# Kernel optimization log

Hardware: AMD Instinct MI355X
Metric: run time of the kernel (lower is better)

Reference implementation:

```python
import jax, jax.numpy as jnp
import numpy as np

K = 3       # kernel size
PAD = 1
IMG = 512   # hard-coded img_size in source
CIN = 32
COUT = 32
B = 1
NORI = 8    # output_stabilizer_size


def make_group_mask(size=IMG, n=NORI):
    # group_conv_8mask: partition image into 8 angular sectors around the
    # fisheye center -> one-hot [8, H, W] mask selecting one orientation per pixel.
    c = (size - 1) / 2.0
    yy, xx = np.meshgrid(np.arange(size), np.arange(size), indexing='ij')
    ang = np.arctan2(yy - c, xx - c)  # [-pi, pi]
    sector = (np.floor((ang + np.pi) / (2.0 * np.pi) * n).astype(np.int64)) % n
    m = np.zeros((n, size, size), np.float32)
    m[sector.reshape(-1), yy.reshape(-1), xx.reshape(-1)] = 1.0
    return m


def rotate_kernel(w, deg):
    # bilinear rotation of [..., K, K] kernel about its center, zero fill (TorchRotate)
    th = np.deg2rad(deg)
    c = (K - 1) / 2.0
    ii, jj = jnp.meshgrid(jnp.arange(K, dtype=jnp.float32), jnp.arange(K, dtype=jnp.float32), indexing='ij')
    cos, sin = np.cos(th).astype(np.float32), np.sin(th).astype(np.float32)
    ys = cos * (ii - c) + sin * (jj - c) + c   # inverse-rotated source coords
    xs = -sin * (ii - c) + cos * (jj - c) + c
    y0 = jnp.floor(ys); x0 = jnp.floor(xs)
    wy = ys - y0; wx = xs - x0
    out = jnp.zeros_like(w)
    for dy, wy_ in ((0, 1.0 - wy), (1, wy)):
        for dx, wx_ in ((0, 1.0 - wx), (1, wx)):
            iy = (y0 + dy).astype(jnp.int32); ix = (x0 + dx).astype(jnp.int32)
            valid = ((iy >= 0) & (iy < K) & (ix >= 0) & (ix < K)).astype(w.dtype)
            iyc = jnp.clip(iy, 0, K - 1); ixc = jnp.clip(ix, 0, K - 1)
            out = out + w[..., iyc, ixc] * (wy_ * wx_ * valid)
    return out


def conv2d(x, w, b):
    y = jax.lax.conv_general_dilated(x, w, (1, 1), ((PAD, PAD), (PAD, PAD)),
                                     dimension_numbers=('NCHW', 'OIHW', 'NCHW'))
    return y + b[None, :, None, None]


def bilinear_gather(x, py, px):
    # x: [Cin, H, W]; py/px: [KK, H, W] fractional sample coords (zero outside)
    H, W = x.shape[-2], x.shape[-1]
    y0 = jnp.floor(py); x0 = jnp.floor(px)
    wy = py - y0; wx = px - x0
    out = jnp.zeros((x.shape[0],) + py.shape, x.dtype)
    for dy, wy_ in ((0, 1.0 - wy), (1, wy)):
        for dx, wx_ in ((0, 1.0 - wx), (1, wx)):
            iy = (y0 + dy).astype(jnp.int32); ix = (x0 + dx).astype(jnp.int32)
            valid = ((iy >= 0) & (iy < H) & (ix >= 0) & (ix < W)).astype(x.dtype)
            iyc = jnp.clip(iy, 0, H - 1); ixc = jnp.clip(ix, 0, W - 1)
            g = x[:, iyc, ixc]  # [Cin, KK, H, W]
            out = out + g * (wy_ * wx_ * valid)[None]
    return out


def _forward(x, weight, offset_w, offset_b, mask_w, mask_b, group_mask):
    # --- group-equivariant weight transform: 8 orientations (0/90/180/270 + 45-rotated set)
    base = weight[:, :, 0]                                        # [Cout, Cin, K, K]
    rots = [jnp.rot90(base, k=r, axes=(-2, -1)) for r in range(4)]
    w45 = rotate_kernel(base, 45.0)
    rots45 = [jnp.rot90(w45, k=r, axes=(-2, -1)) for r in range(4)]
    tw = jnp.stack(rots + rots45, axis=1)                         # [Cout, 8, Cin, K, K]
    tw = tw.reshape(COUT * NORI, CIN, K * K)

    H, W = x.shape[-2], x.shape[-1]
    offset = conv2d(x, offset_w, offset_b)                        # [B, 2*KK, H, W]
    modm = conv2d(x, mask_w, mask_b)                              # [B, KK, H, W]
    offset = offset.at[:, 8:10].set(0.0)                          # center-tap offsets zeroed
    modm = jax.nn.sigmoid(modm.at[:, 4].set(0.0))                 # center-tap logit zeroed

    off = offset.reshape(B, K * K, 2, H, W)                       # (dy, dx) pairs per tap
    ky, kx = jnp.meshgrid(jnp.arange(K, dtype=x.dtype), jnp.arange(K, dtype=x.dtype), indexing='ij')
    py = jnp.arange(H, dtype=x.dtype)[None, :, None] - PAD + ky.reshape(-1, 1, 1)
    px = jnp.arange(W, dtype=x.dtype)[None, None, :] - PAD + kx.reshape(-1, 1, 1)
    py = py[None] + off[:, :, 0]                                  # [B, KK, H, W]
    px = px[None] + off[:, :, 1]

    sampled = jax.vmap(bilinear_gather)(x, py, px)                # [B, Cin, KK, H, W]
    sampled = sampled * modm[:, None]                             # modulation
    y = jnp.einsum('bckhw,ock->bohw', sampled, tw)                # [B, Cout*8, H, W]
    y = y.reshape(B, COUT, NORI, H, W)
    y = jax.nn.relu(y)
    y = y * group_mask[None, None]                                # adaptive pool is identity at stride 1
    return y.sum(axis=2)                                          # [B, Cout, H, W]


def setup_inputs() -> dict:
    key = jax.random.key(0)
    ks = jax.random.split(key, 6)
    stdv = float(1.0 / np.sqrt(CIN * K * K))
    return {
        'input': jax.random.normal(ks[0], (B, CIN, IMG, IMG), jnp.float32),
        'weight': jax.random.uniform(ks[1], (COUT, CIN, 1, K, K), jnp.float32, -stdv, stdv),
        'offset_w': jax.random.normal(ks[2], (2 * K * K, CIN, K, K), jnp.float32) * 0.01,
        'offset_b': jax.random.normal(ks[3], (2 * K * K,), jnp.float32) * 0.01,
        'mask_w': jax.random.normal(ks[4], (K * K, CIN, K, K), jnp.float32) * 0.01,
        'mask_b': jax.random.normal(ks[5], (K * K,), jnp.float32) * 0.01,
        'group_mask': jnp.asarray(make_group_mask()),
    }


def reference(input, weight, offset_w, offset_b, mask_w, mask_b, group_mask):
    return _forward(input, weight, offset_w, offset_b, mask_w, mask_b, group_mask)
```

## Files before the change

kernel.cpp:

```cpp
#include <hip/hip_runtime.h>

#define IMG 512
#define CIN 32
#define COUT 32
#define NORI 8
#define HW (IMG*IMG)

#define TS 16

#define W1 18
#define WR1 19
#define CHS1P 346
#define HALO 4
#define WIN 24
#define WROW 24
#define CHSP 578

typedef _Float16 h2 __attribute__((ext_vector_type(2)));
typedef __fp16  fp16v2 __attribute__((ext_vector_type(2)));
typedef _Float16 f16x8 __attribute__((ext_vector_type(8)));
typedef float    f32x4 __attribute__((ext_vector_type(4)));

__device__ __forceinline__ float dot2acc(unsigned int a, unsigned int b, float c) {
#if __has_builtin(__builtin_amdgcn_fdot2)
    return __builtin_amdgcn_fdot2(__builtin_bit_cast(h2, a),
                                  __builtin_bit_cast(h2, b), c, false);
#else
    h2 av = __builtin_bit_cast(h2, a), bv = __builtin_bit_cast(h2, b);
    return fmaf((float)av[0], (float)bv[0], fmaf((float)av[1], (float)bv[1], c));
#endif
}

__device__ __forceinline__ unsigned int packh2(float a, float b) {
#if __has_builtin(__builtin_amdgcn_cvt_pkrtz)
    fp16v2 r = __builtin_amdgcn_cvt_pkrtz(a, b);
    return __builtin_bit_cast(unsigned int, r);
#else
    h2 r; r[0] = (_Float16)a; r[1] = (_Float16)b;
    return __builtin_bit_cast(unsigned int, r);
#endif
}

__device__ __forceinline__ unsigned int packh2_rne(float a, float b) {
    h2 r; r[0] = (_Float16)a; r[1] = (_Float16)b;
    return __builtin_bit_cast(unsigned int, r);
}

#define GEMV8(TP, S2) do {                                             \
    const uint4* _tp = (TP);                                           \
    _Pragma("unroll")                                                  \
    for (int q = 0; q < 8; ++q) {                                      \
        uint4 u = _tp[q];                                              \
        oacc[q * 4 + 0] = dot2acc((S2), u.x, oacc[q * 4 + 0]);         \
        oacc[q * 4 + 1] = dot2acc((S2), u.y, oacc[q * 4 + 1]);         \
        oacc[q * 4 + 2] = dot2acc((S2), u.z, oacc[q * 4 + 2]);         \
        oacc[q * 4 + 3] = dot2acc((S2), u.w, oacc[q * 4 + 3]);         \
    }                                                                  \
} while (0)

__global__ void build_tw_kernel(const float* __restrict__ weight, unsigned int* __restrict__ tw_h) {
    int idx = blockIdx.x * blockDim.x + threadIdx.x;
    if (idx >= COUT * (CIN / 2)) return;
    int o = idx & 31, cp = idx >> 5;

    float bb[2][9], w45[2][9];
    const float cs = 0.70710678f;
#pragma unroll
    for (int h = 0; h < 2; ++h) {
        int c = 2 * cp + h;
#pragma unroll
        for (int t = 0; t < 9; ++t) bb[h][t] = weight[(o * CIN + c) * 9 + t];
#pragma unroll
        for (int i = 0; i < 3; ++i) {
#pragma unroll
            for (int j = 0; j < 3; ++j) {
                float ys = cs * (float)(i - 1) + cs * (float)(j - 1) + 1.0f;
                float xs = -cs * (float)(i - 1) + cs * (float)(j - 1) + 1.0f;
                float y0f = floorf(ys), x0f = floorf(xs);
                float wy = ys - y0f, wx = xs - x0f;
                int iy0 = (int)y0f, ix0 = (int)x0f;
                float a = 0.0f;
#pragma unroll
                for (int dy = 0; dy < 2; ++dy) {
#pragma unroll
                    for (int dx = 0; dx < 2; ++dx) {
                        int iy = iy0 + dy, ix = ix0 + dx;
                        float wgt = (dy ? wy : 1.0f - wy) * (dx ? wx : 1.0f - wx);
                        bool valid = (iy >= 0) && (iy < 3) && (ix >= 0) && (ix < 3);
                        int iyc = min(max(iy, 0), 2), ixc = min(max(ix, 0), 2);
                        a += bb[h][iyc * 3 + ixc] * (valid ? wgt : 0.0f);
                    }
                }
                w45[h][i * 3 + j] = a;
            }
        }
    }

#pragma unroll
    for (int r = 0; r < NORI; ++r) {
        int rr = r & 3;
#pragma unroll
        for (int i = 0; i < 3; ++i) {
#pragma unroll
            for (int j = 0; j < 3; ++j) {
                int si, sj;
                if (rr == 0) { si = i;     sj = j;     }
                else if (rr == 1) { si = j;     sj = 2 - i; }
                else if (rr == 2) { si = 2 - i; sj = 2 - j; }
                else { si = 2 - j; sj = i;     }
                float v0 = (r < 4) ? bb[0][si * 3 + sj] : w45[0][si * 3 + sj];
                float v1 = (r < 4) ? bb[1][si * 3 + sj] : w45[1][si * 3 + sj];
                tw_h[(((r * 9) + (i * 3 + j)) * (CIN / 2) + cp) * COUT + o] =
                    packh2_rne(v0, v1);
            }
        }
    }
}

__global__ void pack_owmb_kernel(const float* __restrict__ offw, const float* __restrict__ mskw,
                                 unsigned int* __restrict__ owmb) {
    int idx = blockIdx.x * blockDim.x + threadIdx.x;
    if (idx >= 9 * 16 * 32) return;
    int oc = idx & 31;
    int cp = (idx >> 5) & 15;
    int kt = idx >> 9;
    float v0 = 0.0f, v1 = 0.0f;
    if (oc < 18) {
        v0 = offw[(oc * CIN + 2 * cp) * 9 + kt];
        v1 = offw[(oc * CIN + 2 * cp + 1) * 9 + kt];
    } else if (oc < 27) {
        v0 = mskw[((oc - 18) * CIN + 2 * cp) * 9 + kt];
        v1 = mskw[((oc - 18) * CIN + 2 * cp + 1) * 9 + kt];
    }
    owmb[(kt * 16 + cp) * 32 + oc] = packh2_rne(v0, v1);
}

__global__ __launch_bounds__(256, 4) void offset_mask_mfma_kernel(
    const float* __restrict__ x,
    const unsigned int* __restrict__ owmb,
    const float* __restrict__ offb, const float* __restrict__ mskb,
    float* __restrict__ om)
{
    __shared__ unsigned int Lp[16 * CHS1P];

    const int tiles_x = IMG / TS;
    int bid = (int)blockIdx.x;
    bid = (bid % 8) * (1024 / 8) + bid / 8;
    int bx = bid % tiles_x, by = bid / tiles_x;
    int tid = threadIdx.x;
    int y0w = by * TS - 1, x0w = bx * TS - 1;

    for (int i = tid; i < 16 * (W1 * W1); i += 256) {
        int pr = i / (W1 * W1), cell = i % (W1 * W1);
        int rr = cell / W1, cc = cell % W1;
        int gy = y0w + rr, gx = x0w + cc;
        float a = 0.0f, b = 0.0f;
        if ((unsigned)gy < (unsigned)IMG && (unsigned)gx < (unsigned)IMG) {
            const float* x0 = x + (2 * pr) * HW + gy * IMG + gx;
            a = x0[0]; b = x0[HW];
        }
        Lp[pr * CHS1P + rr * WR1 + cc] = packh2_rne(a, b);
    }
    __syncthreads();

    int lane = tid & 63, wid = tid >> 6;
    int lrow = lane & 15, lhi = lane >> 4;

    f32x4 acc[4][2] = {};

#pragma unroll
    for (int kt = 0; kt < 9; ++kt) {
        const int ky = kt / 3, kx = kt % 3;
        const unsigned int* tb = owmb + (kt * 16 + lhi * 4) * 32 + lrow;
        unsigned int bu0[4], bu1[4];
#pragma unroll
        for (int jj = 0; jj < 4; ++jj) {
            bu0[jj] = tb[jj * 32];
            bu1[jj] = tb[jj * 32 + 16];
        }
        uint4 b0q = make_uint4(bu0[0], bu0[1], bu0[2], bu0[3]);
        uint4 b1q = make_uint4(bu1[0], bu1[1], bu1[2], bu1[3]);
        f16x8 bf0 = __builtin_bit_cast(f16x8, b0q);
        f16x8 bf1 = __builtin_bit_cast(f16x8, b1q);

#pragma unroll
        for (int mt = 0; mt < 4; ++mt) {
            int yy = wid * 4 + mt;
            int lq = (yy + ky) * WR1 + (lrow + kx);
            unsigned int au[4];
#pragma unroll
            for (int j = 0; j < 4; ++j)
                au[j] = Lp[(lhi * 4 + j) * CHS1P + lq];
            uint4 aq = make_uint4(au[0], au[1], au[2], au[3]);
            f16x8 af = __builtin_bit_cast(f16x8, aq);
            acc[mt][0] = __builtin_amdgcn_mfma_f32_16x16x32_f16(af, bf0, acc[mt][0], 0, 0, 0);
            acc[mt][1] = __builtin_amdgcn_mfma_f32_16x16x32_f16(af, bf1, acc[mt][1], 0, 0, 0);
        }
    }

    float bias_n0 = offb[lrow];
    float bias_n1 = (lrow < 2) ? offb[16 + lrow]
                  : ((lrow < 11) ? mskb[lrow - 2] : 0.0f);
    int Xs = bx * 16 + lhi * 4;
#pragma unroll
    for (int mt = 0; mt < 4; ++mt) {
        int Yg = by * 16 + wid * 4 + mt;
        {
            int oc = lrow;
            float* op = om + oc * HW + Yg * IMG + Xs;
            bool zero = (oc == 8) || (oc == 9);
#pragma unroll
            for (int q = 0; q < 4; ++q)
                op[q] = zero ? 0.0f : (acc[mt][0][q] + bias_n0);
        }
        {
            int oc = 16 + lrow;
            if (oc < 27) {
                float* op = om + oc * HW + Yg * IMG + Xs;
#pragma unroll
                for (int q = 0; q < 4; ++q) {
                    float t = acc[mt][1][q] + bias_n1;
                    if (oc >= 18) t = (oc == 22) ? 0.5f : 1.0f / (1.0f + __expf(-t));
                    op[q] = t;
                }
            }
        }
    }
}

__global__ __launch_bounds__(256, 4) void deform_mfma_kernel(
    const float* __restrict__ x,
    const float* __restrict__ om,
    const float* __restrict__ gm,
    const unsigned int* __restrict__ tw_h,
    float* __restrict__ out)
{
    __shared__ unsigned int Lx[16 * CHSP];
    __shared__ uint2 Wl[256];
    __shared__ unsigned int LQa[256];
    __shared__ int flags[2];

    const int tiles_x = IMG / TS;
    int bid = (int)blockIdx.x;
    bid = (bid % 8) * (1024 / 8) + bid / 8;
    int bx = bid % tiles_x, by = bid / tiles_x;
    int tid = threadIdx.x;
    int tx = tid & 15, ty = tid >> 4;
    int X = bx * TS + tx, Y = by * TS + ty;
    int p = Y * IMG + X;
    int y0w = by * TS - HALO, x0w = bx * TS - HALO;

    if (tid < 2) flags[tid] = 0;
    __syncthreads();

    for (int i = tid; i < 16 * (WIN * WIN); i += 256) {
        int pr = i / (WIN * WIN), cell = i % (WIN * WIN);
        int rr = cell / WIN, cc = cell % WIN;
        int gy = y0w + rr, gx = x0w + cc;
        float a = 0.0f, b = 0.0f;
        if ((unsigned)gy < (unsigned)IMG && (unsigned)gx < (unsigned)IMG) {
            const float* x0 = x + (2 * pr) * HW + gy * IMG + gx;
            a = x0[0]; b = x0[HW];
        }
        Lx[pr * CHSP + rr * WROW + cc] = packh2_rne(a, b);
    }

    int r = 0;
#pragma unroll
    for (int n = 1; n < NORI; ++n) r = (gm[n * HW + p] > 0.5f) ? n : r;

    bool slow = false;
    for (int kt = 0; kt < 9; ++kt) {
        int ky = kt / 3, kx = kt - ky * 3;
        float offy = om[(2 * kt) * HW + p];
        float offx = om[(2 * kt + 1) * HW + p];
        float pyf = (float)(Y - 1 + ky) + offy;
        float pxf = (float)(X - 1 + kx) + offx;
        int iy0 = (int)floorf(pyf), ix0 = (int)floorf(pxf);
        int ryu = iy0 - y0w, rxu = ix0 - x0w;
        slow |= !(((unsigned)ryu < (WIN - 1)) && ((unsigned)rxu < (WIN - 1)));
    }
    atomicOr(&flags[0], 1 << r);
    if (slow) flags[1] = 1;
    __syncthreads();

    int rmaskv = __builtin_amdgcn_readfirstlane(flags[0]);
    int anyslow = flags[1];

    if (anyslow) {
        float oacc[32];
#pragma unroll
        for (int o = 0; o < 32; ++o) oacc[o] = 0.0f;
        for (int kt = 0; kt < 9; ++kt) {
            int ky = kt / 3, kx = kt - ky * 3;
            float offy = om[(2 * kt) * HW + p];
            float offx = om[(2 * kt + 1) * HW + p];
            float m    = om[(18 + kt) * HW + p];
            float pyf = (float)(Y - 1 + ky) + offy;
            float pxf = (float)(X - 1 + kx) + offx;
            float y0f = floorf(pyf), x0f = floorf(pxf);
            float wy = pyf - y0f, wx = pxf - x0f;
            int iy0 = (int)y0f, ix0 = (int)x0f;
            float vy0 = ((unsigned)iy0 < (unsigned)IMG) ? 1.0f : 0.0f;
            float vy1 = ((unsigned)(iy0 + 1) < (unsigned)IMG) ? 1.0f : 0.0f;
            float vx0 = ((unsigned)ix0 < (unsigned)IMG) ? 1.0f : 0.0f;
            float vx1 = ((unsigned)(ix0 + 1) < (unsigned)IMG) ? 1.0f : 0.0f;
            float w00 = m * (1.0f - wy) * (1.0f - wx) * vy0 * vx0;
            float w01 = m * (1.0f - wy) * wx * vy0 * vx1;
            float w10 = m * wy * (1.0f - wx) * vy1 * vx0;
            float w11 = m * wy * wx * vy1 * vx1;
            int cy0 = min(max(iy0, 0), IMG - 1), cy1 = min(max(iy0 + 1, 0), IMG - 1);
            int cx0 = min(max(ix0, 0), IMG - 1), cx1 = min(max(ix0 + 1, 0), IMG - 1);
            int g00 = cy0 * IMG + cx0, g01 = cy0 * IMG + cx1;
            int g10 = cy1 * IMG + cx0, g11 = cy1 * IMG + cx1;
            const uint4* tp = (const uint4*)(tw_h + (unsigned)((r * 9 + kt) * (CIN / 2)) * COUT);
            for (int cp = 0; cp < CIN / 2; ++cp) {
                const float* xc0 = x + (2 * cp) * HW;
                const float* xc1 = xc0 + HW;
                float s0 = fmaf(w00, xc0[g00], fmaf(w01, xc0[g01],
                           fmaf(w10, xc0[g10], w11 * xc0[g11])));
                float s1 = fmaf(w00, xc1[g00], fmaf(w01, xc1[g01],
                           fmaf(w10, xc1[g10], w11 * xc1[g11])));
                unsigned int s2 = packh2(s0, s1);
                GEMV8(tp + cp * 8, s2);
            }
        }
#pragma unroll
        for (int o = 0; o < 32; ++o) out[o * HW + p] = fmaxf(oacc[o], 0.0f);
        return;
    }

    int lane = tid & 63, wid = tid >> 6;
    int lrow = lane & 15, lhi = lane >> 4;

    f32x4 acc[4][2] = {};

    for (int kt = 0; kt < 9; ++kt) {
        int ky = kt / 3, kx = kt - ky * 3;
        {
            float offy = om[(2 * kt) * HW + p];
            float offx = om[(2 * kt + 1) * HW + p];
            float m    = om[(18 + kt) * HW + p];
            float pyf = (float)(Y - 1 + ky) + offy;
            float pxf = (float)(X - 1 + kx) + offx;
            float y0f = floorf(pyf), x0f = floorf(pxf);
            float wy = pyf - y0f, wx = pxf - x0f;
            int iy0 = (int)y0f, ix0 = (int)x0f;
            float vy0 = ((unsigned)iy0 < (unsigned)IMG) ? 1.0f : 0.0f;
            float vy1 = ((unsigned)(iy0 + 1) < (unsigned)IMG) ? 1.0f : 0.0f;
            float vx0 = ((unsigned)ix0 < (unsigned)IMG) ? 1.0f : 0.0f;
            float vx1 = ((unsigned)(ix0 + 1) < (unsigned)IMG) ? 1.0f : 0.0f;
            float w00 = m * (1.0f - wy) * (1.0f - wx) * vy0 * vx0;
            float w01 = m * (1.0f - wy) * wx * vy0 * vx1;
            float w10 = m * wy * (1.0f - wx) * vy1 * vx0;
            float w11 = m * wy * wx * vy1 * vx1;
            Wl[tid]  = make_uint2(packh2_rne(w00, w01), packh2_rne(w10, w11));
            LQa[tid] = (unsigned)((iy0 - y0w) * WROW + (ix0 - x0w)) | ((unsigned)r << 12);
        }
        __syncthreads();

        int Rv[4];
        unsigned int sam[4][4];
#pragma unroll
        for (int mt = 0; mt < 4; ++mt) {
            int px = (wid * 4 + mt) * 16 + lrow;
            uint2 wv = Wl[px];
            unsigned lqr = LQa[px];
            h2 wpa = __builtin_bit_cast(h2, wv.x);
            h2 wpb = __builtin_bit_cast(h2, wv.y);
            h2 w00 = __builtin_shufflevector(wpa, wpa, 0, 0);
            h2 w01 = __builtin_shufflevector(wpa, wpa, 1, 1);
            h2 w10 = __builtin_shufflevector(wpb, wpb, 0, 0);
            h2 w11 = __builtin_shufflevector(wpb, wpb, 1, 1);
            int lq = (int)(lqr & 0xFFF);
            Rv[mt] = (int)(lqr >> 12);
#pragma unroll
            for (int j = 0; j < 4; ++j) {
                int lb = (lhi * 4 + j) * CHSP + lq;
                h2 v00 = __builtin_bit_cast(h2, Lx[lb]);
                h2 v01 = __builtin_bit_cast(h2, Lx[lb + 1]);
                h2 v10 = __builtin_bit_cast(h2, Lx[lb + WROW]);
                h2 v11 = __builtin_bit_cast(h2, Lx[lb + WROW + 1]);
                h2 s = w00 * v00 + w01 * v01 + w10 * v10 + w11 * v11;
                sam[mt][j] = __builtin_bit_cast(unsigned int, s);
            }
        }

        int rm = rmaskv;
        while (rm) {
            int rr = __ffs(rm) - 1;
            rm &= rm - 1;
            const unsigned int* tb = tw_h +
                (unsigned)((rr * 9 + kt) * (CIN / 2) + lhi * 4) * COUT + lrow;
            unsigned int bu0[4], bu1[4];
#pragma unroll
            for (int jj = 0; jj < 4; ++jj) {
                bu0[jj] = tb[jj * COUT];
                bu1[jj] = tb[jj * COUT + 16];
            }
            uint4 b0q = make_uint4(bu0[0], bu0[1], bu0[2], bu0[3]);
            uint4 b1q = make_uint4(bu1[0], bu1[1], bu1[2], bu1[3]);
            f16x8 bf0 = __builtin_bit_cast(f16x8, b0q);
            f16x8 bf1 = __builtin_bit_cast(f16x8, b1q);

#pragma unroll
            for (int mt = 0; mt < 4; ++mt) {
                unsigned int keep = (Rv[mt] == rr) ? 0xFFFFFFFFu : 0u;
                uint4 aq = make_uint4(sam[mt][0] & keep, sam[mt][1] & keep,
                                      sam[mt][2] & keep, sam[mt][3] & keep);
                f16x8 af = __builtin_bit_cast(f16x8, aq);
                acc[mt][0] = __builtin_amdgcn_mfma_f32_16x16x32_f16(af, bf0, acc[mt][0], 0, 0, 0);
                acc[mt][1] = __builtin_amdgcn_mfma_f32_16x16x32_f16(af, bf1, acc[mt][1], 0, 0, 0);
            }
        }
        __syncthreads();
    }

    int Xs = bx * 16 + lhi * 4;
#pragma unroll
    for (int mt = 0; mt < 4; ++mt) {
        int Yg = by * 16 + wid * 4 + mt;
#pragma unroll
        for (int nt = 0; nt < 2; ++nt) {
            float* op = out + (nt * 16 + lrow) * HW + Yg * IMG + Xs;
#pragma unroll
            for (int q = 0; q < 4; ++q)
                op[q] = fmaxf(acc[mt][nt][q], 0.0f);
        }
    }
}

extern "C" void kernel_launch(void* const* d_in, const int* in_sizes, int n_in,
                              void* d_out, int out_size, void* d_ws, size_t ws_size,
                              hipStream_t stream) {
    const float* x      = (const float*)d_in[0];
    const float* weight = (const float*)d_in[1];
    const float* offw   = (const float*)d_in[2];
    const float* offb   = (const float*)d_in[3];
    const float* mskw   = (const float*)d_in[4];
    const float* mskb   = (const float*)d_in[5];
    const float* gm     = (const float*)d_in[6];
    float* out = (float*)d_out;

    unsigned int* tw_h = (unsigned int*)d_ws;
    unsigned int* owmb = (unsigned int*)((char*)d_ws + 147456);
    float* om = (float*)((char*)d_ws + 294912);

    build_tw_kernel<<<2, 256, 0, stream>>>(weight, tw_h);
    pack_owmb_kernel<<<18, 256, 0, stream>>>(offw, mskw, owmb);

    const int tiles = (IMG / TS) * (IMG / TS);
    offset_mask_mfma_kernel<<<tiles, 256, 0, stream>>>(x, owmb, offb, mskb, om);
    deform_mfma_kernel<<<tiles, 256, 0, stream>>>(x, om, gm, tw_h, out);
}
```

Baseline: 84.10 us.

## Fuse offset/mask conv into deform kernel via shared-memory fp16 buffer

Merges the offset/mask MFMA convolution into the deformable conv kernel. The offset and mask values are computed from the input tile already staged in shared memory, then kept in LDS as fp16 instead of a 27-channel fp32 global buffer. This drops one kernel launch, the global write and read-back of the offset/mask tensor, and the second staging of the input halo. In exchange it uses more LDS per block, lowers launch bounds to 3 blocks per SIMD, and stores offsets at fp16 precision, which could shift sampling coordinates slightly.

```diff
diff --git a/kernel.cpp b/kernel.cpp
--- a/kernel.cpp
+++ b/kernel.cpp
@@ -8,9 +8,6 @@
 
 #define TS 16
 
-#define W1 18
-#define WR1 19
-#define CHS1P 346
 #define HALO 4
 #define WIN 24
 #define WROW 24
@@ -44,6 +41,14 @@
 __device__ __forceinline__ unsigned int packh2_rne(float a, float b) {
     h2 r; r[0] = (_Float16)a; r[1] = (_Float16)b;
     return __builtin_bit_cast(unsigned int, r);
+}
+
+__device__ __forceinline__ unsigned short f16bits(float v) {
+    _Float16 h = (_Float16)v;
+    return __builtin_bit_cast(unsigned short, h);
+}
+__device__ __forceinline__ float f16val(unsigned short u) {
+    return (float)__builtin_bit_cast(_Float16, u);
 }
 
 #define GEMV8(TP, S2) do {                                             \
@@ -135,107 +140,16 @@
     owmb[(kt * 16 + cp) * 32 + oc] = packh2_rne(v0, v1);
 }
 
-__global__ __launch_bounds__(256, 4) void offset_mask_mfma_kernel(
+__global__ __launch_bounds__(256, 3) void fused_deform_kernel(
     const float* __restrict__ x,
     const unsigned int* __restrict__ owmb,
     const float* __restrict__ offb, const float* __restrict__ mskb,
-    float* __restrict__ om)
-{
-    __shared__ unsigned int Lp[16 * CHS1P];
-
-    const int tiles_x = IMG / TS;
-    int bid = (int)blockIdx.x;
-    bid = (bid % 8) * (1024 / 8) + bid / 8;
-    int bx = bid % tiles_x, by = bid / tiles_x;
-    int tid = threadIdx.x;
-    int y0w = by * TS - 1, x0w = bx * TS - 1;
-
-    for (int i = tid; i < 16 * (W1 * W1); i += 256) {
-        int pr = i / (W1 * W1), cell = i % (W1 * W1);
-        int rr = cell / W1, cc = cell % W1;
-        int gy = y0w + rr, gx = x0w + cc;
-        float a = 0.0f, b = 0.0f;
-        if ((unsigned)gy < (unsigned)IMG && (unsigned)gx < (unsigned)IMG) {
-            const float* x0 = x + (2 * pr) * HW + gy * IMG + gx;
-            a = x0[0]; b = x0[HW];
-        }
-        Lp[pr * CHS1P + rr * WR1 + cc] = packh2_rne(a, b);
-    }
-    __syncthreads();
-
-    int lane = tid & 63, wid = tid >> 6;
-    int lrow = lane & 15, lhi = lane >> 4;
-
-    f32x4 acc[4][2] = {};
-
-#pragma unroll
-    for (int kt = 0; kt < 9; ++kt) {
-        const int ky = kt / 3, kx = kt % 3;
-        const unsigned int* tb = owmb + (kt * 16 + lhi * 4) * 32 + lrow;
-        unsigned int bu0[4], bu1[4];
-#pragma unroll
-        for (int jj = 0; jj < 4; ++jj) {
-            bu0[jj] = tb[jj * 32];
-            bu1[jj] = tb[jj * 32 + 16];
-        }
-        uint4 b0q = make_uint4(bu0[0], bu0[1], bu0[2], bu0[3]);
-        uint4 b1q = make_uint4(bu1[0], bu1[1], bu1[2], bu1[3]);
-        f16x8 bf0 = __builtin_bit_cast(f16x8, b0q);
-        f16x8 bf1 = __builtin_bit_cast(f16x8, b1q);
-
-#pragma unroll
-        for (int mt = 0; mt < 4; ++mt) {
-            int yy = wid * 4 + mt;
-            int lq = (yy + ky) * WR1 + (lrow + kx);
-            unsigned int au[4];
-#pragma unroll
-            for (int j = 0; j < 4; ++j)
-                au[j] = Lp[(lhi * 4 + j) * CHS1P + lq];
-            uint4 aq = make_uint4(au[0], au[1], au[2], au[3]);
-            f16x8 af = __builtin_bit_cast(f16x8, aq);
-            acc[mt][0] = __builtin_amdgcn_mfma_f32_16x16x32_f16(af, bf0, acc[mt][0], 0, 0, 0);
-            acc[mt][1] = __builtin_amdgcn_mfma_f32_16x16x32_f16(af, bf1, acc[mt][1], 0, 0, 0);
-        }
-    }
-
-    float bias_n0 = offb[lrow];
-    float bias_n1 = (lrow < 2) ? offb[16 + lrow]
-                  : ((lrow < 11) ? mskb[lrow - 2] : 0.0f);
-    int Xs = bx * 16 + lhi * 4;
-#pragma unroll
-    for (int mt = 0; mt < 4; ++mt) {
-        int Yg = by * 16 + wid * 4 + mt;
-        {
-            int oc = lrow;
-            float* op = om + oc * HW + Yg * IMG + Xs;
-            bool zero = (oc == 8) || (oc == 9);
-#pragma unroll
-            for (int q = 0; q < 4; ++q)
-                op[q] = zero ? 0.0f : (acc[mt][0][q] + bias_n0);
-        }
-        {
-            int oc = 16 + lrow;
-            if (oc < 27) {
-                float* op = om + oc * HW + Yg * IMG + Xs;
-#pragma unroll
-                for (int q = 0; q < 4; ++q) {
-                    float t = acc[mt][1][q] + bias_n1;
-                    if (oc >= 18) t = (oc == 22) ? 0.5f : 1.0f / (1.0f + __expf(-t));
-                    op[q] = t;
-                }
-            }
-        }
-    }
-}
-
-__global__ __launch_bounds__(256, 4) void deform_mfma_kernel(
-    const float* __restrict__ x,
-    const float* __restrict__ om,
     const float* __restrict__ gm,
     const unsigned int* __restrict__ tw_h,
     float* __restrict__ out)
 {
     __shared__ unsigned int Lx[16 * CHSP];
+    __shared__ unsigned short OMl[256 * 27];
     __shared__ uint2 Wl[256];
     __shared__ unsigned int LQa[256];
     __shared__ int flags[2];
@@ -251,7 +165,6 @@
     int y0w = by * TS - HALO, x0w = bx * TS - HALO;
 
     if (tid < 2) flags[tid] = 0;
-    __syncthreads();
 
     for (int i = tid; i < 16 * (WIN * WIN); i += 256) {
         int pr = i / (WIN * WIN), cell = i % (WIN * WIN);
@@ -264,6 +177,74 @@
         }
         Lx[pr * CHSP + rr * WROW + cc] = packh2_rne(a, b);
     }
+    __syncthreads();
+
+    int lane = tid & 63, wid = tid >> 6;
+    int lrow = lane & 15, lhi = lane >> 4;
+
+    {
+        f32x4 acc1[4][2] = {};
+#pragma unroll
+        for (int kt = 0; kt < 9; ++kt) {
+            const int ky = kt / 3, kx = kt % 3;
+            const unsigned int* tb = owmb + (kt * 16 + lhi * 4) * 32 + lrow;
+            unsigned int bu0[4], bu1[4];
+#pragma unroll
+            for (int jj = 0; jj < 4; ++jj) {
+                bu0[jj] = tb[jj * 32];
+                bu1[jj] = tb[jj * 32 + 16];
+            }
+            uint4 b0q = make_uint4(bu0[0], bu0[1], bu0[2], bu0[3]);
+            uint4 b1q = make_uint4(bu1[0], bu1[1], bu1[2], bu1[3]);
+            f16x8 bf0 = __builtin_bit_cast(f16x8, b0q);
+            f16x8 bf1 = __builtin_bit_cast(f16x8, b1q);
+
+#pragma unroll
+            for (int mt = 0; mt < 4; ++mt) {
+                int yy = wid * 4 + mt;
+                int lq1 = (yy + ky + 3) * WROW + (lrow + kx + 3);
+                unsigned int au[4];
+#pragma unroll
+                for (int j = 0; j < 4; ++j)
+                    au[j] = Lx[(lhi * 4 + j) * CHSP + lq1];
+                uint4 aq = make_uint4(au[0], au[1], au[2], au[3]);
+                f16x8 af = __builtin_bit_cast(f16x8, aq);
+                acc1[mt][0] = __builtin_amdgcn_mfma_f32_16x16x32_f16(af, bf0, acc1[mt][0], 0, 0, 0);
+                acc1[mt][1] = __builtin_amdgcn_mfma_f32_16x16x32_f16(af, bf1, acc1[mt][1], 0, 0, 0);
+            }
+        }
+
+        float bias_n0 = offb[lrow];
+        float bias_n1 = (lrow < 2) ? offb[16 + lrow]
+                      : ((lrow < 11) ? mskb[lrow - 2] : 0.0f);
+#pragma unroll
+        for (int mt = 0; mt < 4; ++mt) {
+            int py_l = wid * 4 + mt;
+            {
+                int oc = lrow;
+                bool zero = (oc == 8) || (oc == 9);
+#pragma unroll
+                for (int q = 0; q < 4; ++q) {
+                    int px_l = py_l * 16 + lhi * 4 + q;
+                    float v = zero ? 0.0f : (acc1[mt][0][q] + bias_n0);
+                    OMl[px_l * 27 + oc] = f16bits(v);
+                }
+            }
+            {
+                int oc = 16 + lrow;
+                if (oc < 27) {
+#pragma unroll
+                    for (int q = 0; q < 4; ++q) {
+                        int px_l = py_l * 16 + lhi * 4 + q;
+                        float t = acc1[mt][1][q] + bias_n1;
+                        if (oc >= 18) t = (oc == 22) ? 0.5f : 1.0f / (1.0f + __expf(-t));
+                        OMl[px_l * 27 + oc] = f16bits(t);
+                    }
+                }
+            }
+        }
+    }
+    __syncthreads();
 
     int r = 0;
 #pragma unroll
@@ -272,8 +253,8 @@
     bool slow = false;
     for (int kt = 0; kt < 9; ++kt) {
         int ky = kt / 3, kx = kt - ky * 3;
-        float offy = om[(2 * kt) * HW + p];
-        float offx = om[(2 * kt + 1) * HW + p];
+        float offy = f16val(OMl[tid * 27 + 2 * kt]);
+        float offx = f16val(OMl[tid * 27 + 2 * kt + 1]);
         float pyf = (float)(Y - 1 + ky) + offy;
         float pxf = (float)(X - 1 + kx) + offx;
         int iy0 = (int)floorf(pyf), ix0 = (int)floorf(pxf);
@@ -293,9 +274,9 @@
         for (int o = 0; o < 32; ++o) oacc[o] = 0.0f;
         for (int kt = 0; kt < 9; ++kt) {
             int ky = kt / 3, kx = kt - ky * 3;
-            float offy = om[(2 * kt) * HW + p];
-            float offx = om[(2 * kt + 1) * HW + p];
-            float m    = om[(18 + kt) * HW + p];
+            float offy = f16val(OMl[tid * 27 + 2 * kt]);
+            float offx = f16val(OMl[tid * 27 + 2 * kt + 1]);
+            float m    = f16val(OMl[tid * 27 + 18 + kt]);
             float pyf = (float)(Y - 1 + ky) + offy;
             float pxf = (float)(X - 1 + kx) + offx;
             float y0f = floorf(pyf), x0f = floorf(pxf);
@@ -330,17 +311,14 @@
         return;
     }
 
-    int lane = tid & 63, wid = tid >> 6;
-    int lrow = lane & 15, lhi = lane >> 4;
-
     f32x4 acc[4][2] = {};
 
     for (int kt = 0; kt < 9; ++kt) {
         int ky = kt / 3, kx = kt - ky * 3;
         {
-            float offy = om[(2 * kt) * HW + p];
-            float offx = om[(2 * kt + 1) * HW + p];
-            float m    = om[(18 + kt) * HW + p];
+            float offy = f16val(OMl[tid * 27 + 2 * kt]);
+            float offx = f16val(OMl[tid * 27 + 2 * kt + 1]);
+            float m    = f16val(OMl[tid * 27 + 18 + kt]);
             float pyf = (float)(Y - 1 + ky) + offy;
             float pxf = (float)(X - 1 + kx) + offx;
             float y0f = floorf(pyf), x0f = floorf(pxf);
@@ -444,12 +422,10 @@
 
     unsigned int* tw_h = (unsigned int*)d_ws;
     unsigned int* owmb = (unsigned int*)((char*)d_ws + 147456);
-    float* om = (float*)((char*)d_ws + 294912);
 
     build_tw_kernel<<<2, 256, 0, stream>>>(weight, tw_h);
     pack_owmb_kernel<<<18, 256, 0, stream>>>(offw, mskw, owmb);
 
     const int tiles = (IMG / TS) * (IMG / TS);
-    offset_mask_mfma_kernel<<<tiles, 256, 0, stream>>>(x, owmb, offb, mskb, om);
-    deform_mfma_kernel<<<tiles, 256, 0, stream>>>(x, om, gm, tw_h, out);
-}
+    fused_deform_kernel<<<tiles, 256, 0, stream>>>(x, owmb, offb, mskb, gm, tw_h, out);
+}
```

After: 84.73 us. About the same (+0.8%).
